# Kernel optimization log

Measured on AMD Instinct MI355X. Metric: run time of the kernel, lower is better.

The kernel has to match this reference:

```python
import jax, jax.numpy as jnp
import numpy as np

NEG_INF = -1e12
ALPHA = 0.01  # LeakyReLU slope


def setup_inputs() -> dict:
    key = jax.random.key(0)
    ks = jax.random.split(key, 12)
    K, N, DIN, H1, DOUT, FC1 = 64, 1024, 16, 4, 8, 54
    X = jax.random.normal(ks[0], (K, N, DIN), dtype=jnp.float32)
    adj = jax.random.randint(ks[1], (N, N), 0, 2, dtype=jnp.int32)
    # Xavier-uniform-ish init scale (gain 1.414)
    def xavier(k, shape):
        fan_in, fan_out = shape[0], shape[-1]
        lim = 1.414 * np.sqrt(6.0 / (fan_in + fan_out))
        return jax.random.uniform(k, shape, jnp.float32, -lim, lim)
    W1 = xavier(ks[2], (DIN, H1))
    a1 = xavier(ks[3], (2 * H1, 1))
    W2 = xavier(ks[4], (H1, DOUT))
    a2 = xavier(ks[5], (2 * DOUT, 1))
    fc1_w = xavier(ks[6], (N * DOUT, FC1))
    fc1_b = jnp.zeros((FC1,), jnp.float32)
    out_w = xavier(ks[7], (FC1, N))
    out_b = jnp.zeros((N,), jnp.float32)
    return {"X": X, "adj": adj, "W1": W1, "a1": a1, "W2": W2, "a2": a2,
            "fc1_w": fc1_w, "fc1_b": fc1_b, "out_w": out_w, "out_b": out_b}


def _gat_layer(h_in, adj, W, a):
    # h: [K, N, F]
    h = jnp.matmul(h_in, W)
    Fdim = W.shape[1]
    # concat(h_i, h_j) @ a  ==  (h_i . a[:F]) + (h_j . a[F:])
    f1 = jnp.matmul(h, a[:Fdim, 0])  # [K, N]
    f2 = jnp.matmul(h, a[Fdim:, 0])  # [K, N]
    e = jax.nn.leaky_relu(f1[:, :, None] + f2[:, None, :], ALPHA)  # [K, N, N]
    e = jnp.where(adj[None, :, :] > 0, e, NEG_INF)
    att = jax.nn.softmax(e, axis=2)
    return jnp.einsum('kij,kjf->kif', att, h)


def reference(X, adj, W1, a1, W2, a2, fc1_w, fc1_b, out_w, out_b):
    x = jax.nn.relu(_gat_layer(X, adj, W1, a1))
    x = jax.nn.relu(_gat_layer(x, adj, W2, a2))
    x = x.reshape(x.shape[0], -1)  # [K, N*dim_output]
    x = jax.nn.relu(jnp.matmul(x, fc1_w) + fc1_b)
    return jnp.matmul(x, out_w) + out_b  # [K, N] q-values
```

## Files before the change

kernel.cpp:

```cpp
#include <hip/hip_runtime.h>
#include <hip/hip_bf16.h>

constexpr int K    = 64;
constexpr int N    = 1024;
constexpr int DIN  = 16;
constexpr int H1   = 4;
constexpr int DOUT = 8;
constexpr int FC1  = 54;

#define ALPHA_F   (0.01f)
#define LOG2E_F   (1.4426950408889634f)

typedef unsigned int uint;
typedef short  bf16x8 __attribute__((ext_vector_type(8)));
typedef float  f32x4  __attribute__((ext_vector_type(4)));

__device__ inline float fast_exp2(float x) {
#if __has_builtin(__builtin_amdgcn_exp2f)
    return __builtin_amdgcn_exp2f(x);
#else
    return __expf(x * 0.6931471805599453f);
#endif
}

__device__ inline uint pk_bf16(float a, float b) {
    union { __hip_bfloat162 h; uint u; } v;
    v.h = __float22bfloat162_rn(make_float2(a, b));
    return v.u;
}

__global__ __launch_bounds__(512) void prep_kernel(
        const int* __restrict__ adj, unsigned long long* __restrict__ maskM,
        const float* __restrict__ fc1w, float* __restrict__ wt,
        const float* __restrict__ X, const float* __restrict__ W1,
        const float* __restrict__ a1,
        float* __restrict__ h1, float* __restrict__ f11, float* __restrict__ f21) {
    int b = blockIdx.x;
    if (b < 2048) {
        int wave = threadIdx.x >> 6, lane = threadIdx.x & 63;
        int wid = b * 8 + wave;
        int jw  = wid >> 10;
        int i   = wid & 1023;
        int v = adj[i * N + (jw << 6) + lane];
        unsigned long long m = __ballot(v > 0);
        if (lane == 0) maskM[i * 16 + jw] = m;
    } else if (b < 2112) {
        __shared__ float tile[128 * FC1];
        const int m0 = (b - 2048) * 128;
        const float* src = fc1w + (size_t)m0 * FC1;
        for (int idx = threadIdx.x; idx < 128 * FC1; idx += 512)
            tile[idx] = src[idx];
        __syncthreads();
        for (int idx = threadIdx.x; idx < 128 * FC1; idx += 512) {
            int c = idx >> 7, mm = idx & 127;
            wt[(size_t)c * (N * DOUT) + m0 + mm] = tile[mm * FC1 + c];
        }
    } else {
        int idx = (b - 2112) * 512 + threadIdx.x;
        const float4* x4 = (const float4*)(X + (size_t)idx * DIN);
        float h[H1] = {0.f, 0.f, 0.f, 0.f};
        #pragma unroll
        for (int q = 0; q < 4; q++) {
            float4 xv = x4[q];
            #pragma unroll
            for (int f = 0; f < H1; f++) {
                h[f] += xv.x * W1[(q * 4 + 0) * H1 + f] + xv.y * W1[(q * 4 + 1) * H1 + f]
                      + xv.z * W1[(q * 4 + 2) * H1 + f] + xv.w * W1[(q * 4 + 3) * H1 + f];
            }
        }
        float s1 = 0.f, s2 = 0.f;
        #pragma unroll
        for (int f = 0; f < H1; f++) { s1 += h[f] * a1[f]; s2 += h[f] * a1[H1 + f]; }
        *(float4*)(h1 + (size_t)idx * H1) = make_float4(h[0], h[1], h[2], h[3]);
        f11[idx] = s1 * LOG2E_F;
        f21[idx] = s2 * LOG2E_F;
    }
}

template <int F, bool FUSE>
__global__ __launch_bounds__(512, 4) void gat_attn_mfma(
        const unsigned long long* __restrict__ maskM,
        const float* __restrict__ h,
        const float* __restrict__ f1,
        const float* __restrict__ f2,
        const float* __restrict__ W2,
        const float* __restrict__ a2,
        float* __restrict__ o_x,
        float* __restrict__ o_f1,
        float* __restrict__ o_f2) {
    __shared__ uint4 HB[2048];
    __shared__ float F2s[1024];
    __shared__ float XP[8][16][5];

    const int tid  = threadIdx.x;
    const int lane = tid & 63;
    const int wv   = tid >> 6;
    const int quad = lane >> 4;
    const int n16  = lane & 15;
    const int k    = blockIdx.x >> 3;

    {
        const float* hk = h + (size_t)k * N * F;
        #pragma unroll
        for (int e = tid; e < 2048; e += 512) {
            int c = e >> 6, l = e & 63, q = l >> 4, n = l & 15;
            uint4 dw;
            if (n < F) {
                const float* hp = hk + (size_t)(c * 32 + q * 8) * F + n;
                dw.x = pk_bf16(hp[0],     hp[F]);
                dw.y = pk_bf16(hp[2 * F], hp[3 * F]);
                dw.z = pk_bf16(hp[4 * F], hp[5 * F]);
                dw.w = pk_bf16(hp[6 * F], hp[7 * F]);
            } else if (n == F) {
                dw = make_uint4(0x3f803f80u, 0x3f803f80u, 0x3f803f80u, 0x3f803f80u);
            } else {
                dw = make_uint4(0u, 0u, 0u, 0u);
            }
            HB[e] = dw;
        }
        if (tid < 256)
            ((float4*)F2s)[tid] = ((const float4*)(f2 + k * N))[tid];
    }
    __syncthreads();

    const int itile = (blockIdx.x & 7) * 8 + wv;
    const int ibase = itile * 16;
    const int irow  = ibase + n16;
    const float f1v = f1[k * N + irow];
    const uint4* mrow = (const uint4*)((const char*)maskM + (size_t)irow * 128);

    f32x4 acc = {0.f, 0.f, 0.f, 0.f};
    union { bf16x8 v; uint u[4]; } af;
    union { bf16x8 v; uint4 q; }  bfrag;

    #pragma unroll 2
    for (int g = 0; g < 8; g++) {
        const uint4 Mg = mrow[g];
        #pragma unroll
        for (int cc = 0; cc < 4; cc++) {
            const int c = g * 4 + cc;
            const uint mdw = (cc == 0) ? Mg.x : (cc == 1) ? Mg.y
                           : (cc == 2) ? Mg.z : Mg.w;
            const uint mb  = (mdw >> (quad * 8)) & 0xffu;
            float4 fa = *(const float4*)(F2s + c * 32 + quad * 8);
            float4 fb = *(const float4*)(F2s + c * 32 + quad * 8 + 4);
            bfrag.q = HB[c * 64 + lane];
            float f2e[8] = {fa.x, fa.y, fa.z, fa.w, fb.x, fb.y, fb.z, fb.w};
            float pv[8];
            #pragma unroll
            for (int jj = 0; jj < 8; jj++) {
                float x = f1v + f2e[jj];
                float e = fmaxf(x, ALPHA_F * x);
                float p = fast_exp2(e);
                pv[jj] = (mb & (1u << jj)) ? p : 0.f;
            }
            #pragma unroll
            for (int pr = 0; pr < 4; pr++)
                af.u[pr] = pk_bf16(pv[2 * pr], pv[2 * pr + 1]);
            acc = __builtin_amdgcn_mfma_f32_16x16x32_bf16(af.v, bfrag.v, acc, 0, 0, 0);
        }
    }

    #pragma unroll
    for (int r = 0; r < 4; r++) {
        float den = __shfl(acc[r], (lane & 48) + F);
        float inv = (den > 0.f) ? 1.f / den : 0.f;
        float xo  = fmaxf(acc[r] * inv, 0.f);
        int m = quad * 4 + r;
        if constexpr (FUSE) {
            if (n16 < F) XP[wv][m][n16] = xo;
        } else {
            if (n16 < F) o_x[((size_t)k * N + ibase + m) * F + n16] = xo;
        }
    }

    if constexpr (FUSE) {
        __syncthreads();
        if (lane < 16) {
            int m = lane;
            float x0 = XP[wv][m][0], x1 = XP[wv][m][1];
            float x2v = XP[wv][m][2], x3 = XP[wv][m][3];
            float hv[DOUT];
            #pragma unroll
            for (int f = 0; f < DOUT; f++) {
                hv[f] = x0 * W2[f]      + x1 * W2[8 + f]
                      + x2v * W2[16 + f] + x3 * W2[24 + f];
            }
            float t1 = 0.f, t2 = 0.f;
            #pragma unroll
            for (int f = 0; f < DOUT; f++) { t1 += hv[f] * a2[f]; t2 += hv[f] * a2[DOUT + f]; }
            const int row = k * N + ibase + m;
            float* op = o_x + (size_t)row * DOUT;
            *(float4*)op       = make_float4(hv[0], hv[1], hv[2], hv[3]);
            *(float4*)(op + 4) = make_float4(hv[4], hv[5], hv[6], hv[7]);
            o_f1[row] = t1 * LOG2E_F;
            o_f2[row] = t2 * LOG2E_F;
        }
    }
}

__global__ __launch_bounds__(256) void fc1_kernel(
        const float* __restrict__ x2, const float* __restrict__ wt,
        const float* __restrict__ b, float* __restrict__ y) {
    const int bid  = blockIdx.x;
    const int k    = bid / FC1;
    const int c    = bid - k * FC1;
    const int wave = threadIdx.x >> 6;
    const int lane = threadIdx.x & 63;
    const float4* x4 = (const float4*)(x2 + (size_t)k * N * DOUT) + wave * 512 + lane;
    const float4* w4 = (const float4*)(wt + (size_t)c * N * DOUT) + wave * 512 + lane;
    float s0 = 0.f, s1 = 0.f;
    #pragma unroll
    for (int q = 0; q < 8; q += 2) {
        float4 a0 = x4[q * 64],      w0 = w4[q * 64];
        float4 a1 = x4[q * 64 + 64], w1 = w4[q * 64 + 64];
        s0 += a0.x * w0.x + a0.y * w0.y + a0.z * w0.z + a0.w * w0.w;
        s1 += a1.x * w1.x + a1.y * w1.y + a1.z * w1.z + a1.w * w1.w;
    }
    float s = s0 + s1;
    #pragma unroll
    for (int off = 32; off > 0; off >>= 1) s += __shfl_xor(s, off);
    __shared__ float red[4];
    if (lane == 0) red[wave] = s;
    __syncthreads();
    if (threadIdx.x == 0)
        y[bid] = fmaxf(red[0] + red[1] + red[2] + red[3] + b[c], 0.f);
}

__global__ void fc2_kernel(const float* __restrict__ y,
                           const float* __restrict__ out_w,
                           const float* __restrict__ out_b,
                           float* __restrict__ out) {
    int n = blockIdx.x * blockDim.x + threadIdx.x;
    int k = blockIdx.y;
    const float* yk = y + (size_t)k * FC1;
    float s = out_b[n];
    #pragma unroll 6
    for (int c = 0; c < FC1; c++) s += yk[c] * out_w[(size_t)c * N + n];
    out[(size_t)k * N + n] = s;
}

extern "C" void kernel_launch(void* const* d_in, const int* in_sizes, int n_in,
                              void* d_out, int out_size, void* d_ws, size_t ws_size,
                              hipStream_t stream) {
    const float* X     = (const float*)d_in[0];
    const int*   adj   = (const int*)  d_in[1];
    const float* W1    = (const float*)d_in[2];
    const float* a1    = (const float*)d_in[3];
    const float* W2    = (const float*)d_in[4];
    const float* a2    = (const float*)d_in[5];
    const float* fc1w  = (const float*)d_in[6];
    const float* fc1b  = (const float*)d_in[7];
    const float* outw  = (const float*)d_in[8];
    const float* outb  = (const float*)d_in[9];
    float* out = (float*)d_out;

    float* ws  = (float*)d_ws;
    float* h1  = ws;
    float* f11 = h1  + 262144;
    float* f21 = f11 + 65536;
    float* h2  = f21 + 65536;
    float* f12 = h2  + 524288;
    float* f22 = f12 + 65536;
    float* x2  = f22 + 65536;
    float* y   = x2  + 524288;
    float* wt  = y   + 4096;
    unsigned long long* mM = (unsigned long long*)(wt + 442368);

    prep_kernel<<<dim3(2240), dim3(512), 0, stream>>>(
        adj, mM, fc1w, wt, X, W1, a1, h1, f11, f21);

    gat_attn_mfma<4, true><<<dim3(K * 8), dim3(512), 0, stream>>>(
        mM, h1, f11, f21, W2, a2, h2, f12, f22);

    gat_attn_mfma<8, false><<<dim3(K * 8), dim3(512), 0, stream>>>(
        mM, h2, f12, f22, nullptr, nullptr, x2, nullptr, nullptr);

    fc1_kernel<<<dim3(K * FC1), dim3(256), 0, stream>>>(x2, wt, fc1b, y);
    fc2_kernel<<<dim3(N / 256, K), dim3(256), 0, stream>>>(y, outw, outb, out);
}
```

Measured before the change: 139.3 us.

## Produce pre-packed bf16 MFMA B-fragments upstream and read them from global

The producers (prep kernel and the fused first GAT layer) now write h directly in the packed bf16 MFMA B-operand layout with the ones column for the denominator. The attention kernels no longer rebuild this 32KB LDS tile per block and instead read fragments straight from global/L2. This removes the per-block repack and its LDS footprint, which may raise occupancy. The cost is that B-fragment loads in the inner loop now go to global memory rather than LDS, with added latency.

```diff
diff --git a/kernel.cpp b/kernel.cpp
--- a/kernel.cpp
+++ b/kernel.cpp
@@ -29,12 +29,13 @@
     return v.u;
 }
 
+
 __global__ __launch_bounds__(512) void prep_kernel(
         const int* __restrict__ adj, unsigned long long* __restrict__ maskM,
         const float* __restrict__ fc1w, float* __restrict__ wt,
         const float* __restrict__ X, const float* __restrict__ W1,
         const float* __restrict__ a1,
-        float* __restrict__ h1, float* __restrict__ f11, float* __restrict__ f21) {
+        uint4* __restrict__ HB1, float* __restrict__ f11, float* __restrict__ f21) {
     int b = blockIdx.x;
     if (b < 2048) {
         int wave = threadIdx.x >> 6, lane = threadIdx.x & 63;
@@ -56,41 +57,67 @@
             wt[(size_t)c * (N * DOUT) + m0 + mm] = tile[mm * FC1 + c];
         }
     } else {
-        int idx = (b - 2112) * 512 + threadIdx.x;
+        __shared__ float hrow[512 * 4];
+        const int bb  = b - 2112;
+        const int k   = bb >> 1;
+        const int j0  = (bb & 1) * 512;
+        const int tid = threadIdx.x;
+        const int idx = k * N + j0 + tid;
         const float4* x4 = (const float4*)(X + (size_t)idx * DIN);
-        float h[H1] = {0.f, 0.f, 0.f, 0.f};
+        float hv_[H1] = {0.f, 0.f, 0.f, 0.f};
         #pragma unroll
         for (int q = 0; q < 4; q++) {
             float4 xv = x4[q];
             #pragma unroll
             for (int f = 0; f < H1; f++) {
-                h[f] += xv.x * W1[(q * 4 + 0) * H1 + f] + xv.y * W1[(q * 4 + 1) * H1 + f]
-                      + xv.z * W1[(q * 4 + 2) * H1 + f] + xv.w * W1[(q * 4 + 3) * H1 + f];
+                hv_[f] += xv.x * W1[(q * 4 + 0) * H1 + f] + xv.y * W1[(q * 4 + 1) * H1 + f]
+                        + xv.z * W1[(q * 4 + 2) * H1 + f] + xv.w * W1[(q * 4 + 3) * H1 + f];
             }
         }
         float s1 = 0.f, s2 = 0.f;
         #pragma unroll
-        for (int f = 0; f < H1; f++) { s1 += h[f] * a1[f]; s2 += h[f] * a1[H1 + f]; }
-        *(float4*)(h1 + (size_t)idx * H1) = make_float4(h[0], h[1], h[2], h[3]);
+        for (int f = 0; f < H1; f++) { s1 += hv_[f] * a1[f]; s2 += hv_[f] * a1[H1 + f]; }
         f11[idx] = s1 * LOG2E_F;
         f21[idx] = s2 * LOG2E_F;
+        #pragma unroll
+        for (int f = 0; f < H1; f++) hrow[tid * 4 + f] = hv_[f];
+        __syncthreads();
+        uint4* HBk = HB1 + (size_t)k * 2048 + (j0 >> 5) * 64;
+        #pragma unroll
+        for (int e = tid; e < 1024; e += 512) {
+            int cl = e >> 6, l = e & 63, q = (l >> 4), n = l & 15;
+            uint4 dw;
+            if (n < H1) {
+                const float* hp = hrow + (cl * 32 + q * 8) * 4 + n;
+                dw.x = pk_bf16(hp[0],  hp[4]);
+                dw.y = pk_bf16(hp[8],  hp[12]);
+                dw.z = pk_bf16(hp[16], hp[20]);
+                dw.w = pk_bf16(hp[24], hp[28]);
+            } else if (n == H1) {
+                dw = make_uint4(0x3f803f80u, 0x3f803f80u, 0x3f803f80u, 0x3f803f80u);
+            } else {
+                dw = make_uint4(0u, 0u, 0u, 0u);
+            }
+            HBk[cl * 64 + l] = dw;
+        }
     }
 }
 
 template <int F, bool FUSE>
 __global__ __launch_bounds__(512, 4) void gat_attn_mfma(
         const unsigned long long* __restrict__ maskM,
-        const float* __restrict__ h,
+        const uint4* __restrict__ HBin,
         const float* __restrict__ f1,
         const float* __restrict__ f2,
         const float* __restrict__ W2,
         const float* __restrict__ a2,
+        uint4* __restrict__ HBout,
         float* __restrict__ o_x,
         float* __restrict__ o_f1,
         float* __restrict__ o_f2) {
-    __shared__ uint4 HB[2048];
     __shared__ float F2s[1024];
-    __shared__ float XP[8][16][5];
+    __shared__ float XPa[8][16][5];
+    __shared__ float XPb[8][16][9];
 
     const int tid  = threadIdx.x;
     const int lane = tid & 63;
@@ -99,28 +126,8 @@
     const int n16  = lane & 15;
     const int k    = blockIdx.x >> 3;
 
-    {
-        const float* hk = h + (size_t)k * N * F;
-        #pragma unroll
-        for (int e = tid; e < 2048; e += 512) {
-            int c = e >> 6, l = e & 63, q = l >> 4, n = l & 15;
-            uint4 dw;
-            if (n < F) {
-                const float* hp = hk + (size_t)(c * 32 + q * 8) * F + n;
-                dw.x = pk_bf16(hp[0],     hp[F]);
-                dw.y = pk_bf16(hp[2 * F], hp[3 * F]);
-                dw.z = pk_bf16(hp[4 * F], hp[5 * F]);
-                dw.w = pk_bf16(hp[6 * F], hp[7 * F]);
-            } else if (n == F) {
-                dw = make_uint4(0x3f803f80u, 0x3f803f80u, 0x3f803f80u, 0x3f803f80u);
-            } else {
-                dw = make_uint4(0u, 0u, 0u, 0u);
-            }
-            HB[e] = dw;
-        }
-        if (tid < 256)
-            ((float4*)F2s)[tid] = ((const float4*)(f2 + k * N))[tid];
-    }
+    if (tid < 256)
+        ((float4*)F2s)[tid] = ((const float4*)(f2 + k * N))[tid];
     __syncthreads();
 
     const int itile = (blockIdx.x & 7) * 8 + wv;
@@ -128,6 +135,7 @@
     const int irow  = ibase + n16;
     const float f1v = f1[k * N + irow];
     const uint4* mrow = (const uint4*)((const char*)maskM + (size_t)irow * 128);
+    const uint4* HBk  = HBin + (size_t)k * 2048;
 
     f32x4 acc = {0.f, 0.f, 0.f, 0.f};
     union { bf16x8 v; uint u[4]; } af;
@@ -144,7 +152,7 @@
             const uint mb  = (mdw >> (quad * 8)) & 0xffu;
             float4 fa = *(const float4*)(F2s + c * 32 + quad * 8);
             float4 fb = *(const float4*)(F2s + c * 32 + quad * 8 + 4);
-            bfrag.q = HB[c * 64 + lane];
+            bfrag.q = HBk[c * 64 + lane];
             float f2e[8] = {fa.x, fa.y, fa.z, fa.w, fb.x, fb.y, fb.z, fb.w};
             float pv[8];
             #pragma unroll
@@ -168,7 +176,7 @@
         float xo  = fmaxf(acc[r] * inv, 0.f);
         int m = quad * 4 + r;
         if constexpr (FUSE) {
-            if (n16 < F) XP[wv][m][n16] = xo;
+            if (n16 < F) XPa[wv][m][n16] = xo;
         } else {
             if (n16 < F) o_x[((size_t)k * N + ibase + m) * F + n16] = xo;
         }
@@ -177,9 +185,9 @@
     if constexpr (FUSE) {
         __syncthreads();
         if (lane < 16) {
-            int m = lane;
-            float x0 = XP[wv][m][0], x1 = XP[wv][m][1];
-            float x2v = XP[wv][m][2], x3 = XP[wv][m][3];
+            const int m = lane;
+            float x0 = XPa[wv][m][0], x1 = XPa[wv][m][1];
+            float x2v = XPa[wv][m][2], x3 = XPa[wv][m][3];
             float hv[DOUT];
             #pragma unroll
             for (int f = 0; f < DOUT; f++) {
@@ -190,11 +198,30 @@
             #pragma unroll
             for (int f = 0; f < DOUT; f++) { t1 += hv[f] * a2[f]; t2 += hv[f] * a2[DOUT + f]; }
             const int row = k * N + ibase + m;
-            float* op = o_x + (size_t)row * DOUT;
-            *(float4*)op       = make_float4(hv[0], hv[1], hv[2], hv[3]);
-            *(float4*)(op + 4) = make_float4(hv[4], hv[5], hv[6], hv[7]);
             o_f1[row] = t1 * LOG2E_F;
             o_f2[row] = t2 * LOG2E_F;
+            #pragma unroll
+            for (int f = 0; f < DOUT; f++) XPb[wv][m][f] = hv[f];
+        }
+        __syncthreads();
+        if (lane < 32) {
+            const int c2    = ibase >> 5;
+            const int qhalf = (ibase >> 4) & 1;
+            const int ql    = lane >> 4;
+            const int n     = lane & 15;
+            const int q     = qhalf * 2 + ql;
+            uint4 dw;
+            if (n < DOUT) {
+                dw.x = pk_bf16(XPb[wv][ql * 8 + 0][n], XPb[wv][ql * 8 + 1][n]);
+                dw.y = pk_bf16(XPb[wv][ql * 8 + 2][n], XPb[wv][ql * 8 + 3][n]);
+                dw.z = pk_bf16(XPb[wv][ql * 8 + 4][n], XPb[wv][ql * 8 + 5][n]);
+                dw.w = pk_bf16(XPb[wv][ql * 8 + 6][n], XPb[wv][ql * 8 + 7][n]);
+            } else if (n == DOUT) {
+                dw = make_uint4(0x3f803f80u, 0x3f803f80u, 0x3f803f80u, 0x3f803f80u);
+            } else {
+                dw = make_uint4(0u, 0u, 0u, 0u);
+            }
+            HBout[(size_t)k * 2048 + c2 * 64 + q * 16 + n] = dw;
         }
     }
 }
@@ -256,25 +283,25 @@
     float* out = (float*)d_out;
 
     float* ws  = (float*)d_ws;
-    float* h1  = ws;
-    float* f11 = h1  + 262144;
+    float* f11 = ws;
     float* f21 = f11 + 65536;
-    float* h2  = f21 + 65536;
-    float* f12 = h2  + 524288;
+    float* f12 = f21 + 65536;
     float* f22 = f12 + 65536;
     float* x2  = f22 + 65536;
     float* y   = x2  + 524288;
     float* wt  = y   + 4096;
     unsigned long long* mM = (unsigned long long*)(wt + 442368);
+    uint4* HB1 = (uint4*)(wt + 442368 + 32768);
+    uint4* HB2 = HB1 + 131072;
 
     prep_kernel<<<dim3(2240), dim3(512), 0, stream>>>(
-        adj, mM, fc1w, wt, X, W1, a1, h1, f11, f21);
+        adj, mM, fc1w, wt, X, W1, a1, HB1, f11, f21);
 
     gat_attn_mfma<4, true><<<dim3(K * 8), dim3(512), 0, stream>>>(
-        mM, h1, f11, f21, W2, a2, h2, f12, f22);
+        mM, HB1, f11, f21, W2, a2, HB2, nullptr, f12, f22);
 
     gat_attn_mfma<8, false><<<dim3(K * 8), dim3(512), 0, stream>>>(
-        mM, h2, f12, f22, nullptr, nullptr, x2, nullptr, nullptr);
+        mM, HB2, f12, f22, nullptr, nullptr, nullptr, x2, nullptr, nullptr);
 
     fc1_kernel<<<dim3(K * FC1), dim3(256), 0, stream>>>(x2, wt, fc1b, y);
     fc2_kernel<<<dim3(N / 256, K), dim3(256), 0, stream>>>(y, outw, outb, out);
```

Measured after the change: 134.7 us. 1.03x faster.
